# Optimization experiments

Hardware: AMD Instinct MI355X
Metric: run time of the kernel (lower is better)

The kernel has to match this reference:

```python
import jax, jax.numpy as jnp
from jax import lax
import numpy as np

RADIUS = 0.1
NSAMPLE = 32
STRIDE = 3
ED_NSAMPLE = 10


def _sqdist(a, b):
    # a: [B,M,3], b: [B,N,3] -> [B,M,N] squared euclidean distance
    return (jnp.sum(a * a, -1)[:, :, None] + jnp.sum(b * b, -1)[:, None, :]
            - 2.0 * jnp.einsum('bmc,bnc->bmn', a, b))


def setup_inputs() -> dict:
    key = jax.random.key(0)
    ks = jax.random.split(key, 16)
    B, N = 8, 4096
    s = 0.05
    inp = {
        'data': jax.random.normal(ks[0], (B, N, 3), dtype=jnp.float32),
        'numpoints': N,
        # stem MLP 3 -> 64
        'W_stem': jax.random.normal(ks[1], (3, 64), dtype=jnp.float32) * s,
        'b_stem': jnp.zeros((64,), jnp.float32),
        # SA shared MLP (3 dp + 64 fj) -> 128
        'W_sa': jax.random.normal(ks[2], (67, 128), dtype=jnp.float32) * s,
        'b_sa': jnp.zeros((128,), jnp.float32),
        # FP MLP (128 interp + 64 skip) -> 64
        'W_fp': jax.random.normal(ks[3], (192, 64), dtype=jnp.float32) * s,
        'b_fp': jnp.zeros((64,), jnp.float32),
        # eigen-feature MLP 3 -> 4 -> 4
        'W_e1': jax.random.normal(ks[4], (3, 4), dtype=jnp.float32) * s,
        'b_e1': jnp.zeros((4,), jnp.float32),
        'W_e2': jax.random.normal(ks[5], (4, 4), dtype=jnp.float32) * s,
        'b_e2': jnp.zeros((4,), jnp.float32),
        # conv_final 1x1: 68 -> 64, + BN affine
        'W_fin': jax.random.normal(ks[6], (68, 64), dtype=jnp.float32) * s,
        'b_fin': jnp.zeros((64,), jnp.float32),
        'gamma': jnp.ones((64,), jnp.float32),
        'beta': jnp.zeros((64,), jnp.float32),
    }
    return inp


def reference(data, numpoints, W_stem, b_stem, W_sa, b_sa, W_fp, b_fp,
              W_e1, b_e1, W_e2, b_e2, W_fin, b_fin, gamma, beta):
    B, N, _ = data.shape
    b_ix = jnp.arange(B)[:, None, None]

    # ---------- encoder: stem MLP ----------
    f0 = jax.nn.relu(data @ W_stem + b_stem)  # [B,N,64]

    # set abstraction: stride-subsample centers, ball query, dp_fj, MLP, max
    sub_idx = jnp.arange(0, N, STRIDE)
    new_xyz = data[:, sub_idx]                 # [B,M,3]
    d2 = _sqdist(new_xyz, data)                # [B,M,N]
    col = jnp.arange(N, dtype=jnp.int32)
    valid = d2 < RADIUS * RADIUS
    keys = jnp.where(valid, col, N + col)      # first-valid ball query ordering
    negk, _ = lax.top_k(-keys, NSAMPLE)
    idx = -negk                                # [B,M,ns]
    first = idx[..., :1]                       # self point always valid
    idx = jnp.where(idx >= N, first, idx)
    g_xyz = data[b_ix, idx]                    # [B,M,ns,3]
    dp = (g_xyz - new_xyz[:, :, None, :]) / RADIUS  # normalize_dp
    g_f = f0[b_ix, idx]                        # [B,M,ns,64]
    feat = jnp.concatenate([dp, g_f], -1)      # [B,M,ns,67]
    h = jax.nn.relu(feat @ W_sa + b_sa)        # [B,M,ns,128]
    f_sub = jnp.max(h, axis=2)                 # [B,M,128]

    # ---------- decoder: 3-NN inverse-distance feature propagation ----------
    d2f = _sqdist(data, new_xyz)               # [B,N,M]
    negd, nn = lax.top_k(-d2f, 3)
    w = 1.0 / (-negd + 1e-8)
    w = w / jnp.sum(w, -1, keepdims=True)      # [B,N,3]
    nbr_f = f_sub[b_ix, nn]                    # [B,N,3,128]
    interp = jnp.einsum('bnk,bnkc->bnc', w, nbr_f)
    f = jax.nn.relu(jnp.concatenate([interp, f0], -1) @ W_fp + b_fp)  # [B,N,64]

    # ---------- KNN covariance eigen-features ----------
    d2e = _sqdist(data, data)                  # [B,N,N]
    _, gidx = lax.top_k(-d2e, ED_NSAMPLE)      # [B,N,k]
    nbr = data[b_ix, gidx]                     # [B,N,k,3]
    cen = nbr - jnp.mean(nbr, axis=2, keepdims=True)
    cov = jnp.einsum('bnkc,bnkd->bncd', cen, cen) / ED_NSAMPLE  # [B,N,3,3]
    eig = jnp.linalg.eigvalsh(cov)             # [B,N,3] ascending
    ef = jax.nn.relu(eig @ W_e1 + b_e1) @ W_e2 + b_e2  # [B,N,4]

    # ---------- fused 1x1 conv + BN (training-mode stats) + relu ----------
    z_in = jnp.concatenate([f, ef], -1)        # [B,N,68]
    zc = z_in @ W_fin + b_fin                  # [B,N,64]
    mu = jnp.mean(zc, axis=(0, 1))
    var = jnp.var(zc, axis=(0, 1))
    z = jax.nn.relu((zc - mu) * lax.rsqrt(var + 1e-5) * gamma + beta)
    z = jnp.transpose(z, (0, 2, 1))            # [B,64,N]
    return (data, z)
```

## Files before the change

### kernel.cpp

```cpp
#include <hip/hip_runtime.h>
#include <stdint.h>

#define BB 8
#define NN 4096
#define MM 1366
#define NS 32
#define RAD2 0.01f
#define NGRP 64
#define KW 8

__device__ __forceinline__ float rl(float v, int l) {
    return __int_as_float(__builtin_amdgcn_readlane(__float_as_int(v), l));
}
__device__ __forceinline__ uint32_t um(uint32_t a, uint32_t b) { return a < b ? a : b; }
__device__ __forceinline__ uint32_t ux(uint32_t a, uint32_t b) { return a > b ? a : b; }
__device__ __forceinline__ uint32_t um3(uint32_t a, uint32_t b, uint32_t c) { return um(um(a, b), c); }

__device__ __forceinline__ void mrg2(uint32_t* kk, uint32_t s0, uint32_t s1) {
    uint32_t n0 = um(kk[0], s0);
    uint32_t n1 = um3(kk[1], ux(kk[0], s0), s1);
    uint32_t n2 = um3(kk[2], ux(kk[1], s0), ux(kk[0], s1));
    uint32_t n3 = um3(kk[3], ux(kk[2], s0), ux(kk[1], s1));
    uint32_t n4 = um3(kk[4], ux(kk[3], s0), ux(kk[2], s1));
    uint32_t n5 = um3(kk[5], ux(kk[4], s0), ux(kk[3], s1));
    uint32_t n6 = um3(kk[6], ux(kk[5], s0), ux(kk[4], s1));
    uint32_t n7 = um3(kk[7], ux(kk[6], s0), ux(kk[5], s1));
    uint32_t n8 = um3(kk[8], ux(kk[7], s0), ux(kk[6], s1));
    uint32_t n9 = um3(kk[9], ux(kk[8], s0), ux(kk[7], s1));
    kk[0]=n0; kk[1]=n1; kk[2]=n2; kk[3]=n3; kk[4]=n4;
    kk[5]=n5; kk[6]=n6; kk[7]=n7; kk[8]=n8; kk[9]=n9;
}

__device__ __forceinline__ void mrg4(uint32_t* kk, uint32_t s0, uint32_t s1,
                                     uint32_t s2, uint32_t s3) {
    uint32_t n0 = um(kk[0], s0);
    uint32_t n1 = um3(kk[1], ux(kk[0], s0), s1);
    uint32_t n2 = um(um3(kk[2], ux(kk[1], s0), ux(kk[0], s1)), s2);
    uint32_t n3 = um3(um3(kk[3], ux(kk[2], s0), ux(kk[1], s1)), ux(kk[0], s2), s3);
    uint32_t n4 = um3(um3(kk[4], ux(kk[3], s0), ux(kk[2], s1)), ux(kk[1], s2), ux(kk[0], s3));
    uint32_t n5 = um3(um3(kk[5], ux(kk[4], s0), ux(kk[3], s1)), ux(kk[2], s2), ux(kk[1], s3));
    uint32_t n6 = um3(um3(kk[6], ux(kk[5], s0), ux(kk[4], s1)), ux(kk[3], s2), ux(kk[2], s3));
    uint32_t n7 = um3(um3(kk[7], ux(kk[6], s0), ux(kk[5], s1)), ux(kk[4], s2), ux(kk[3], s3));
    uint32_t n8 = um3(um3(kk[8], ux(kk[7], s0), ux(kk[6], s1)), ux(kk[5], s2), ux(kk[4], s3));
    uint32_t n9 = um3(um3(kk[9], ux(kk[8], s0), ux(kk[7], s1)), ux(kk[6], s2), ux(kk[5], s3));
    kk[0]=n0; kk[1]=n1; kk[2]=n2; kk[3]=n3; kk[4]=n4;
    kk[5]=n5; kk[6]=n6; kk[7]=n7; kk[8]=n8; kk[9]=n9;
}

__device__ __forceinline__ void srt4(uint32_t& a, uint32_t& b, uint32_t& c, uint32_t& d) {
    uint32_t t0 = um(a, b), t1 = ux(a, b), t2 = um(c, d), t3 = ux(c, d);
    uint32_t s0 = um(t0, t2), m0 = ux(t0, t2), m1 = um(t1, t3), s3 = ux(t1, t3);
    a = s0; b = um(m0, m1); c = ux(m0, m1); d = s3;
}

__device__ __forceinline__ uint32_t spr3(uint32_t v) {
    v = (v | (v << 4)) & 0xC3u;
    v = (v | (v << 2)) & 0x249u;
    return v;
}

__global__ __launch_bounds__(256) void k_stem(const float* __restrict__ data,
                                              const float* __restrict__ Ws,
                                              const float* __restrict__ bs,
                                              float* __restrict__ f0,
                                              float* __restrict__ out,
                                              float4* __restrict__ cand4) {
    int blk = blockIdx.x;
    if (blk >= (BB * NN * 64) / 256) {
        int t = (blk - (BB * NN * 64) / 256) * 256 + threadIdx.x;
        float x = data[t * 3], y = data[t * 3 + 1], z = data[t * 3 + 2];
        out[t * 3] = x; out[t * 3 + 1] = y; out[t * 3 + 2] = z;
        cand4[t] = make_float4(x, y, z, x * x + y * y + z * z);
        return;
    }
    int t = blk * 256 + threadIdx.x;
    int c = t & 63;
    int r = t >> 6;
    const float* d = data + r * 3;
    float acc = bs[c];
    acc = fmaf(d[0], Ws[c], acc);
    acc = fmaf(d[1], Ws[64 + c], acc);
    acc = fmaf(d[2], Ws[128 + c], acc);
    f0[t] = fmaxf(acc, 0.f);
}

__global__ __launch_bounds__(256) void k_sort(const float4* __restrict__ cand4,
                                              float4* __restrict__ cand4s,
                                              uint32_t* __restrict__ perm,
                                              float4* __restrict__ gbox) {
    __shared__ uint32_t cnt[4096];
    __shared__ uint32_t part[256];
    int b = blockIdx.x, t = threadIdx.x;
    const float4* cb = cand4 + b * NN;
    for (int i = t; i < 4096; i += 256) cnt[i] = 0;
    __syncthreads();
    uint32_t cid[16];
    #pragma unroll
    for (int u = 0; u < 16; ++u) {
        float4 c = cb[u * 256 + t];
        int ix = (int)floorf((c.x + 4.f) * 2.f);
        int iy = (int)floorf((c.y + 4.f) * 2.f);
        int iz = (int)floorf((c.z + 4.f) * 2.f);
        ix = ix < 0 ? 0 : (ix > 15 ? 15 : ix);
        iy = iy < 0 ? 0 : (iy > 15 ? 15 : iy);
        iz = iz < 0 ? 0 : (iz > 15 ? 15 : iz);
        uint32_t m = spr3((uint32_t)ix) | (spr3((uint32_t)iy) << 1) | (spr3((uint32_t)iz) << 2);
        cid[u] = m;
        atomicAdd(&cnt[m], 1u);
    }
    __syncthreads();
    uint32_t c16[16];
    uint32_t s = 0;
    #pragma unroll
    for (int u = 0; u < 16; ++u) { c16[u] = cnt[t * 16 + u]; s += c16[u]; }
    part[t] = s;
    __syncthreads();
    for (int off = 1; off < 256; off <<= 1) {
        uint32_t v = (t >= off) ? part[t - off] : 0u;
        __syncthreads();
        part[t] += v;
        __syncthreads();
    }
    uint32_t run = part[t] - s;
    #pragma unroll
    for (int u = 0; u < 16; ++u) { cnt[t * 16 + u] = run; run += c16[u]; }
    __syncthreads();
    #pragma unroll
    for (int u = 0; u < 16; ++u) {
        int p = u * 256 + t;
        uint32_t pos = atomicAdd(&cnt[cid[u]], 1u);
        cand4s[b * NN + pos] = cb[p];
        perm[b * NN + pos] = (uint32_t)p;
    }
    __syncthreads();
    if (t < NGRP) {
        float4 mn = make_float4(1e30f, 1e30f, 1e30f, 0.f);
        float4 mx = make_float4(-1e30f, -1e30f, -1e30f, 0.f);
        for (int j = 0; j < 64; ++j) {
            float4 c = cand4s[b * NN + t * 64 + j];
            mn.x = fminf(mn.x, c.x); mn.y = fminf(mn.y, c.y); mn.z = fminf(mn.z, c.z);
            mx.x = fmaxf(mx.x, c.x); mx.y = fmaxf(mx.y, c.y); mx.z = fmaxf(mx.z, c.z);
        }
        gbox[(b * NGRP + t) * 2]     = mn;
        gbox[(b * NGRP + t) * 2 + 1] = mx;
    }
}

__global__ __launch_bounds__(512) void k_knn(const float4* __restrict__ cand4s,
                                             const uint32_t* __restrict__ perm,
                                             const float4* __restrict__ gbox,
                                             uint32_t* __restrict__ mrg) {
    __shared__ float4 sBox[2 * NGRP];
    __shared__ uint32_t sKK[KW - 1][64][10];
    int t = threadIdx.x, w = t >> 6, lane = t & 63;
    int gw = blockIdx.x;
    int b = gw >> 6;
    int g = gw & (NGRP - 1);
    for (int i = t; i < 2 * NGRP; i += 512) sBox[i] = gbox[b * 2 * NGRP + i];
    __syncthreads();
    const float4* cs = cand4s + b * NN;
    const uint32_t* ps = perm + b * NN;
    float4 me = cs[g * 64 + lane];
    uint32_t mo = ps[g * 64 + lane];
    float px = me.x, py = me.y, pz = me.z, pa = me.w;
    uint32_t kk[10];
    #pragma unroll
    for (int r = 0; r < 10; ++r) kk[r] = 0xFFFFFF00u + r;

    auto scan_packets = [&](int jg, uint32_t thrC) {
        const float4* cp = cs + jg * 64;
        const uint4* pq = (const uint4*)(ps + jg * 64);
        uint32_t thr = um(kk[9], thrC);
        for (int j = 0; j < 16; ++j) {
            float4 ca  = cp[j * 4];
            float4 cbv = cp[j * 4 + 1];
            float4 cc  = cp[j * 4 + 2];
            float4 cd  = cp[j * 4 + 3];
            uint4 pm = pq[j];
            float da  = fmaxf(fmaf(-2.f, fmaf(pz, ca.z,  fmaf(py, ca.y,  px * ca.x)),  pa + ca.w),  0.f);
            float db_ = fmaxf(fmaf(-2.f, fmaf(pz, cbv.z, fmaf(py, cbv.y, px * cbv.x)), pa + cbv.w), 0.f);
            float dc  = fmaxf(fmaf(-2.f, fmaf(pz, cc.z,  fmaf(py, cc.y,  px * cc.x)),  pa + cc.w),  0.f);
            float dd  = fmaxf(fmaf(-2.f, fmaf(pz, cd.z,  fmaf(py, cd.y,  px * cd.x)),  pa + cd.w),  0.f);
            uint32_t ka = (__float_as_uint(da)  & 0xFFFFF000u) | pm.x;
            uint32_t kb = (__float_as_uint(db_) & 0xFFFFF000u) | pm.y;
            uint32_t kc = (__float_as_uint(dc)  & 0xFFFFF000u) | pm.z;
            uint32_t kd = (__float_as_uint(dd)  & 0xFFFFF000u) | pm.w;
            uint32_t mn4 = um(um(ka, kb), um(kc, kd));
            if (__ballot(mn4 < thr)) {
                srt4(ka, kb, kc, kd);
                mrg4(kk, ka, kb, kc, kd);
                thr = um(kk[9], thrC);
            }
        }
    };

    scan_packets(g, 0xFFFFFFFFu);

    uint32_t thrK = (kk[9] & 0xFFFFF000u) + 0x1000u;

    if (w > 0) {
        #pragma unroll
        for (int r = 0; r < 10; ++r) kk[r] = 0xFFFFFF00u + r;
    }

    for (int jg = w; jg < NGRP; jg += KW) {
        if (jg == g) continue;
        float4 bmn = sBox[jg * 2], bmx = sBox[jg * 2 + 1];
        float dx = fmaxf(fmaxf(bmn.x - px, px - bmx.x), 0.f);
        float dy = fmaxf(fmaxf(bmn.y - py, py - bmx.y), 0.f);
        float dz = fmaxf(fmaxf(bmn.z - pz, pz - bmx.z), 0.f);
        float lb = fmaf(dx, dx, fmaf(dy, dy, dz * dz));
        uint32_t mt = um(kk[9], thrK);
        float tf = __uint_as_float((mt & 0xFFFFF000u) + 0x1000u) * 1.0005f;
        if (__ballot(lb < tf))
            scan_packets(jg, thrK);
    }

    if (w > 0) {
        #pragma unroll
        for (int r = 0; r < 10; ++r) sKK[w - 1][lane][r] = kk[r];
    }
    __syncthreads();
    if (w == 0) {
        for (int ww = 0; ww < KW - 1; ++ww) {
            uint32_t s[10];
            #pragma unroll
            for (int r = 0; r < 10; ++r) s[r] = sKK[ww][lane][r];
            mrg4(kk, s[0], s[1], s[2], s[3]);
            mrg4(kk, s[4], s[5], s[6], s[7]);
            mrg2(kk, s[8], s[9]);
        }
        int gp = b * NN + (int)mo;
        #pragma unroll
        for (int r = 0; r < 10; ++r) mrg[r * (BB * NN) + gp] = kk[r];
    }
}

__device__ __forceinline__ void jrot(float& app, float& aqq, float& apq,
                                     float& arp, float& arq) {
    float ap = apq;
    if (fabsf(ap) > 1e-32f) {
        float th = (aqq - app) / (2.f * ap);
        float t = 1.f / (fabsf(th) + sqrtf(th * th + 1.f));
        t = th < 0.f ? -t : t;
        float c = 1.f / sqrtf(t * t + 1.f);
        float s = t * c;
        app = app - t * ap;
        aqq = aqq + t * ap;
        apq = 0.f;
        float rp = arp, rq = arq;
        arp = c * rp - s * rq;
        arq = s * rp + c * rq;
    }
}

__global__ __launch_bounds__(256) void k_knn_eig(const float4* __restrict__ cand4,
                                                 const uint32_t* __restrict__ mrg,
                                                 const float* __restrict__ We1,
                                                 const float* __restrict__ be1,
                                                 const float* __restrict__ We2,
                                                 const float* __restrict__ be2,
                                                 float* __restrict__ ef) {
    int t = blockIdx.x * 256 + threadIdx.x;
    int b = t >> 12;
    const float4* cb = cand4 + b * NN;
    uint32_t kk[10];
    #pragma unroll
    for (int r = 0; r < 10; ++r) kk[r] = mrg[r * (BB * NN) + t];
    float xs[10], ys[10], zs[10];
    float mx = 0.f, my = 0.f, mz = 0.f;
    #pragma unroll
    for (int r = 0; r < 10; ++r) {
        int n = (int)(kk[r] & 0xFFFu);
        float4 cr = cb[n];
        xs[r] = cr.x; ys[r] = cr.y; zs[r] = cr.z;
        mx += xs[r]; my += ys[r]; mz += zs[r];
    }
    mx *= 0.1f; my *= 0.1f; mz *= 0.1f;
    float a00 = 0, a01 = 0, a02 = 0, a11 = 0, a12 = 0, a22 = 0;
    #pragma unroll
    for (int r = 0; r < 10; ++r) {
        float x = xs[r] - mx, y = ys[r] - my, z = zs[r] - mz;
        a00 = fmaf(x, x, a00); a01 = fmaf(x, y, a01); a02 = fmaf(x, z, a02);
        a11 = fmaf(y, y, a11); a12 = fmaf(y, z, a12); a22 = fmaf(z, z, a22);
    }
    a00 *= 0.1f; a01 *= 0.1f; a02 *= 0.1f; a11 *= 0.1f; a12 *= 0.1f; a22 *= 0.1f;
    #pragma unroll
    for (int sweep = 0; sweep < 6; ++sweep) {
        jrot(a00, a11, a01, a02, a12);
        jrot(a00, a22, a02, a01, a12);
        jrot(a11, a22, a12, a01, a02);
    }
    float e0 = a00, e1 = a11, e2 = a22, tmp;
    if (e0 > e1) { tmp = e0; e0 = e1; e1 = tmp; }
    if (e1 > e2) { tmp = e1; e1 = e2; e2 = tmp; }
    if (e0 > e1) { tmp = e0; e0 = e1; e1 = tmp; }
    float tt[4];
    #pragma unroll
    for (int i = 0; i < 4; ++i) {
        float v = be1[i];
        v = fmaf(e0, We1[i], v);
        v = fmaf(e1, We1[4 + i], v);
        v = fmaf(e2, We1[8 + i], v);
        tt[i] = fmaxf(v, 0.f);
    }
    #pragma unroll
    for (int i = 0; i < 4; ++i) {
        float v = be2[i];
        v = fmaf(tt[0], We2[i], v);
        v = fmaf(tt[1], We2[4 + i], v);
        v = fmaf(tt[2], We2[8 + i], v);
        v = fmaf(tt[3], We2[12 + i], v);
        ef[t * 4 + i] = v;
    }
}

__global__ __launch_bounds__(256) void k_sa(const float4* __restrict__ cand4,
                                            const float* __restrict__ data,
                                            const float* __restrict__ f0,
                                            const uint32_t* __restrict__ mrg,
                                            const float* __restrict__ Wsa,
                                            const float* __restrict__ bsa,
                                            float* __restrict__ fsub) {
    __shared__ float2 sW[67 * 64];
    __shared__ int sIdx[4][NS];
    for (int i = threadIdx.x; i < 67 * 64; i += 256) {
        int k = i >> 6, c = i & 63;
        sW[i] = make_float2(Wsa[k * 128 + c], Wsa[k * 128 + 64 + c]);
    }
    __syncthreads();
    int wv = threadIdx.x >> 6, lane = threadIdx.x & 63;
    int gm = blockIdx.x * 4 + wv;
    if (gm >= BB * MM) return;
    int b = gm / MM, m = gm - b * MM;
    const float4* cb4 = cand4 + b * NN;
    const float* db = data + b * NN * 3;
    float4 cen = cb4[3 * m];
    float cx = cen.x, cy = cen.y, cz = cen.z, sa = cen.w;

    int cnt;
    bool fallback;
    {
        float d2l = 1e30f;
        int idxl = 0;
        if (lane < 10) {
            uint32_t key = mrg[lane * (BB * NN) + b * NN + 3 * m];
            idxl = (int)(key & 0xFFFu);
            float4 c = cb4[idxl];
            float dot = fmaf(cz, c.z, fmaf(cy, c.y, cx * c.x));
            d2l = (sa + c.w) - 2.f * dot;
        }
        bool valid = (lane < 10) && (d2l < RAD2);
        unsigned long long mask = __ballot(valid);
        if (valid) sIdx[wv][__popcll(mask & ((1ull << lane) - 1ull))] = idxl;
        cnt = __popcll(mask);
        fallback = rl(d2l, 9) < RAD2 * 1.0005f;
    }
    if (fallback) {
        cnt = 0;
        for (int base = 0; base < NN; base += 64) {
            int n = base + lane;
            float4 c = cb4[n];
            float dot = fmaf(cz, c.z, fmaf(cy, c.y, cx * c.x));
            float d2 = (sa + c.w) - 2.f * dot;
            bool valid = d2 < RAD2;
            unsigned long long mask = __ballot(valid);
            if (valid) {
                int pos = cnt + __popcll(mask & ((1ull << lane) - 1ull));
                if (pos < NS) sIdx[wv][pos] = n;
            }
            cnt += __popcll(mask);
            if (cnt >= NS) break;
        }
    }
    int scnt = cnt < NS ? cnt : NS;

    float cl = lane == 0 ? cx : (lane == 1 ? cy : cz);
    float hb0 = bsa[lane], hb1 = bsa[64 + lane];
    float m0 = 0.f, m1 = 0.f;

    for (int s0 = 0; s0 < scnt; s0 += 4) {
        float fr[4], fr2[4];
        #pragma unroll
        for (int u = 0; u < 4; ++u) {
            int s = s0 + u;
            if (s >= scnt) s = 0;
            int nj = sIdx[wv][s];
            int fb = (b * NN + nj) * 64;
            float v;
            if (lane >= 3) v = f0[fb + lane - 3];
            else           v = (db[nj * 3 + lane] - cl) * 10.0f;
            fr[u] = v;
            fr2[u] = (lane < 3) ? f0[fb + 61 + lane] : 0.f;
        }
        float h0[4], h1[4];
        #pragma unroll
        for (int u = 0; u < 4; ++u) { h0[u] = hb0; h1[u] = hb1; }
        for (int k = 0; k < 64; ++k) {
            float2 w = sW[k * 64 + lane];
            #pragma unroll
            for (int u = 0; u < 4; ++u) {
                float fv = rl(fr[u], k);
                h0[u] = fmaf(fv, w.x, h0[u]);
                h1[u] = fmaf(fv, w.y, h1[u]);
            }
        }
        #pragma unroll
        for (int k = 64; k < 67; ++k) {
            float2 w = sW[k * 64 + lane];
            #pragma unroll
            for (int u = 0; u < 4; ++u) {
                float fv = rl(fr2[u], k - 64);
                h0[u] = fmaf(fv, w.x, h0[u]);
                h1[u] = fmaf(fv, w.y, h1[u]);
            }
        }
        #pragma unroll
        for (int u = 0; u < 4; ++u) {
            m0 = fmaxf(m0, fmaxf(h0[u], 0.f));
            m1 = fmaxf(m1, fmaxf(h1[u], 0.f));
        }
    }
    fsub[gm * 128 + lane] = m0;
    fsub[gm * 128 + 64 + lane] = m1;
}

__global__ __launch_bounds__(512) void k_interp(const float4* __restrict__ cand4,
                                                const float* __restrict__ fsub,
                                                float* __restrict__ itp) {
    __shared__ float4 sC[MM];
    __shared__ float sMD[8][64][3];
    __shared__ int   sMI[8][64][3];
    __shared__ float sWts[64][3];
    __shared__ int   sNbr[64][3];
    int t = threadIdx.x, wv = t >> 6, lane = t & 63;
    int blk = blockIdx.x;
    int b = blk >> 6;
    int pbase = (blk & 63) * 64;
    const float4* cb4 = cand4 + b * NN;
    for (int m = t; m < MM; m += 512) sC[m] = cb4[3 * m];
    __syncthreads();
    int p = pbase + lane;
    float4 pm = cb4[p];
    float px = pm.x, py = pm.y, pz = pm.z, pa = pm.w;
    float d0 = 1e30f, d1 = 1e30f, d2v = 1e30f;
    int n0 = 0, n1 = 0, n2 = 0;
    int ms = wv * 171, me = ms + 171 < MM ? ms + 171 : MM;
    for (int m = ms; m < me; ++m) {
        float4 c = sC[m];
        float dd = (pa + c.w) - 2.f * (px * c.x + py * c.y + pz * c.z);
        if (dd < d2v) {
            if (dd < d1) {
                d2v = d1; n2 = n1;
                if (dd < d0) { d1 = d0; n1 = n0; d0 = dd; n0 = m; }
                else         { d1 = dd; n1 = m; }
            } else { d2v = dd; n2 = m; }
        }
    }
    sMD[wv][lane][0] = d0; sMD[wv][lane][1] = d1; sMD[wv][lane][2] = d2v;
    sMI[wv][lane][0] = n0; sMI[wv][lane][1] = n1; sMI[wv][lane][2] = n2;
    __syncthreads();
    if (wv == 0) {
        d0 = sMD[0][lane][0]; d1 = sMD[0][lane][1]; d2v = sMD[0][lane][2];
        n0 = sMI[0][lane][0]; n1 = sMI[0][lane][1]; n2 = sMI[0][lane][2];
        for (int w = 1; w < 8; ++w) {
            #pragma unroll
            for (int r = 0; r < 3; ++r) {
                float dd = sMD[w][lane][r];
                int mm = sMI[w][lane][r];
                if (dd < d2v) {
                    if (dd < d1) {
                        d2v = d1; n2 = n1;
                        if (dd < d0) { d1 = d0; n1 = n0; d0 = dd; n0 = mm; }
                        else         { d1 = dd; n1 = mm; }
                    } else { d2v = dd; n2 = mm; }
                }
            }
        }
        float w0 = 1.f / (d0 + 1e-8f), w1 = 1.f / (d1 + 1e-8f), w2 = 1.f / (d2v + 1e-8f);
        float ws = w0 + w1 + w2;
        sWts[lane][0] = w0 / ws; sWts[lane][1] = w1 / ws; sWts[lane][2] = w2 / ws;
        sNbr[lane][0] = n0; sNbr[lane][1] = n1; sNbr[lane][2] = n2;
    }
    __syncthreads();
    for (int i = wv * 8; i < wv * 8 + 8; ++i) {
        float a0 = sWts[i][0], a1 = sWts[i][1], a2 = sWts[i][2];
        const float* r0 = fsub + (b * MM + sNbr[i][0]) * 128;
        const float* r1 = fsub + (b * MM + sNbr[i][1]) * 128;
        const float* r2 = fsub + (b * MM + sNbr[i][2]) * 128;
        float v0 = fmaf(a2, r2[lane], fmaf(a1, r1[lane], a0 * r0[lane]));
        float v1 = fmaf(a2, r2[64 + lane], fmaf(a1, r1[64 + lane], a0 * r0[64 + lane]));
        int row = b * NN + pbase + i;
        itp[row * 128 + lane] = v0;
        itp[row * 128 + 64 + lane] = v1;
    }
}

__global__ __launch_bounds__(256) void k_fp(const float* __restrict__ itp,
                                            const float* __restrict__ f0,
                                            const float* __restrict__ W,
                                            const float* __restrict__ bias,
                                            float* __restrict__ outf) {
    __shared__ float sW[192 * 64];
    for (int i = threadIdx.x; i < 192 * 64; i += 256) sW[i] = W[i];
    __syncthreads();
    int lane = threadIdx.x & 63;
    int wv = threadIdx.x >> 6;
    float bb = bias[lane];
    int rowbase = blockIdx.x * 64 + wv * 16;
    for (int it = 0; it < 4; ++it) {
        int r = rowbase + it * 4;
        float fa[4], fbv[4], fc[4], acc[4];
        #pragma unroll
        for (int u = 0; u < 4; ++u) {
            fa[u]  = itp[(r + u) * 128 + lane];
            fbv[u] = itp[(r + u) * 128 + 64 + lane];
            fc[u]  = f0[(r + u) * 64 + lane];
            acc[u] = bb;
        }
        #pragma unroll
        for (int k = 0; k < 192; ++k) {
            float w = sW[k * 64 + lane];
            #pragma unroll
            for (int u = 0; u < 4; ++u) {
                float fv = k < 64 ? rl(fa[u], k)
                         : (k < 128 ? rl(fbv[u], k - 64) : rl(fc[u], k - 128));
                acc[u] = fmaf(fv, w, acc[u]);
            }
        }
        #pragma unroll
        for (int u = 0; u < 4; ++u)
            outf[(r + u) * 64 + lane] = fmaxf(acc[u], 0.f);
    }
}

__global__ __launch_bounds__(256) void k_fin(const float* __restrict__ fb,
                                             const float* __restrict__ efb,
                                             const float* __restrict__ W,
                                             const float* __restrict__ bias,
                                             float* __restrict__ zc) {
    __shared__ float sW[68 * 64];
    for (int i = threadIdx.x; i < 68 * 64; i += 256) sW[i] = W[i];
    __syncthreads();
    int lane = threadIdx.x & 63;
    int wv = threadIdx.x >> 6;
    float bb = bias[lane];
    int rowbase = blockIdx.x * 64 + wv * 16;
    for (int it = 0; it < 4; ++it) {
        int r = rowbase + it * 4;
        float fa[4], fe[4], acc[4];
        #pragma unroll
        for (int u = 0; u < 4; ++u) {
            fa[u] = fb[(r + u) * 64 + lane];
            fe[u] = (lane < 4) ? efb[(r + u) * 4 + lane] : 0.f;
            acc[u] = bb;
        }
        #pragma unroll
        for (int k = 0; k < 68; ++k) {
            float w = sW[k * 64 + lane];
            #pragma unroll
            for (int u = 0; u < 4; ++u) {
                float fv = k < 64 ? rl(fa[u], k) : rl(fe[u], k - 64);
                acc[u] = fmaf(fv, w, acc[u]);
            }
        }
        #pragma unroll
        for (int u = 0; u < 4; ++u)
            zc[(r + u) * 64 + lane] = acc[u];
    }
}

__global__ __launch_bounds__(256) void k_stats1(const float* __restrict__ zc,
                                                float* __restrict__ pp) {
    int t = threadIdx.x;
    int c = t & 63, r4 = t >> 6;
    float s = 0.f, sq = 0.f;
    int base = blockIdx.x * 512;
    for (int i = 0; i < 128; ++i) {
        float v = zc[(base + i * 4 + r4) * 64 + c];
        s += v;
        sq = fmaf(v, v, sq);
    }
    __shared__ float ls[256], lq[256];
    ls[t] = s; lq[t] = sq;
    __syncthreads();
    if (t < 64) {
        float st = ls[t] + ls[t + 64] + ls[t + 128] + ls[t + 192];
        float qt = lq[t] + lq[t + 64] + lq[t + 128] + lq[t + 192];
        pp[blockIdx.x * 128 + t] = st;
        pp[blockIdx.x * 128 + 64 + t] = qt;
    }
}

__global__ __launch_bounds__(64) void k_stats2(const float* __restrict__ pp,
                                               const float* __restrict__ gamma,
                                               const float* __restrict__ beta,
                                               float* __restrict__ ss) {
    int c = threadIdx.x;
    float s = 0.f, sq = 0.f;
    for (int k = 0; k < 64; ++k) {
        s += pp[k * 128 + c];
        sq += pp[k * 128 + 64 + c];
    }
    const float inv = 1.f / (float)(BB * NN);
    float mu = s * inv;
    float var = sq * inv - mu * mu;
    float sc = gamma[c] / sqrtf(var + 1e-5f);
    ss[c] = sc;
    ss[64 + c] = beta[c] - mu * sc;
}

__global__ __launch_bounds__(256) void k_norm_t(const float* __restrict__ zc,
                                                const float* __restrict__ ss,
                                                float* __restrict__ out) {
    __shared__ float sT[64][65];
    int blk = blockIdx.x;
    int b = blk >> 6;
    int nbase = (blk & 63) * 64;
    int c = threadIdx.x & 63;
    int r4 = threadIdx.x >> 6;
    float sc = ss[c], sh = ss[64 + c];
    #pragma unroll
    for (int i = 0; i < 16; ++i) {
        int nr = i * 4 + r4;
        float v = zc[(b * NN + nbase + nr) * 64 + c];
        sT[nr][c] = fmaxf(fmaf(v, sc, sh), 0.f);
    }
    __syncthreads();
    int nn = threadIdx.x & 63;
    #pragma unroll
    for (int i = 0; i < 16; ++i) {
        int cc = i * 4 + r4;
        out[BB * NN * 3 + (b * 64 + cc) * NN + nbase + nn] = sT[nn][cc];
    }
}

extern "C" void kernel_launch(void* const* d_in, const int* in_sizes, int n_in,
                              void* d_out, int out_size, void* d_ws, size_t ws_size,
                              hipStream_t stream) {
    const float* data = (const float*)d_in[0];
    const float* Wst  = (const float*)d_in[2];
    const float* bst  = (const float*)d_in[3];
    const float* Wsa  = (const float*)d_in[4];
    const float* bsa  = (const float*)d_in[5];
    const float* Wfp  = (const float*)d_in[6];
    const float* bfp  = (const float*)d_in[7];
    const float* We1  = (const float*)d_in[8];
    const float* be1  = (const float*)d_in[9];
    const float* We2  = (const float*)d_in[10];
    const float* be2  = (const float*)d_in[11];
    const float* Wfin = (const float*)d_in[12];
    const float* bfin = (const float*)d_in[13];
    const float* gamma = (const float*)d_in[14];
    const float* beta  = (const float*)d_in[15];
    float* out = (float*)d_out;

    float* f0   = (float*)d_ws;
    float* fsub = f0 + 2097152;
    float* efb  = fsub + 1398784;
    float* zc   = efb + 131072;
    float* ss   = zc + 2097152;
    float* pp   = ss + 128;
    float4* cand4 = (float4*)(pp + 8192);
    uint32_t* mrgb = (uint32_t*)((float*)cand4 + 131072);
    float* itp  = (float*)mrgb + 1310720;
    float* fb   = itp + 4194304;
    float4*   cand4s = (float4*)itp;
    uint32_t* perm   = (uint32_t*)(itp + 131072);
    float4*   gbox   = (float4*)(itp + 131072 + 32768);

    k_stem<<<(BB * NN * 64) / 256 + (BB * NN) / 256, 256, 0, stream>>>(
        data, Wst, bst, f0, out, cand4);
    k_sort<<<BB, 256, 0, stream>>>(cand4, cand4s, perm, gbox);
    k_knn<<<BB * NGRP, 512, 0, stream>>>(cand4s, perm, gbox, mrgb);
    k_knn_eig<<<(BB * NN) / 256, 256, 0, stream>>>(cand4, mrgb, We1, be1, We2, be2, efb);
    k_sa<<<(BB * MM + 3) / 4, 256, 0, stream>>>(cand4, data, f0, mrgb, Wsa, bsa, fsub);
    k_interp<<<BB * 64, 512, 0, stream>>>(cand4, fsub, itp);
    k_fp<<<512, 256, 0, stream>>>(itp, f0, Wfp, bfp, fb);
    k_fin<<<512, 256, 0, stream>>>(fb, efb, Wfin, bfin, zc);
    k_stats1<<<64, 256, 0, stream>>>(zc, pp);
    k_stats2<<<1, 64, 0, stream>>>(pp, gamma, beta, ss);
    k_norm_t<<<512, 256, 0, stream>>>(zc, ss, out);
}
```

Measured before the change: 317.8 us.

## Split KNN into home-group pass and independent slice scans merged in eig kernel

The single 512-thread KNN kernel is split into three stages. A 64-thread kernel scans each point's home group and stores a pruning threshold. A scan kernel then runs twice as many 256-thread blocks, each wave handling one of eight slices of the other groups. A final merge of the per-slice top-10 lists moves into the eigen kernel, with the scatter back to original order done there. This removes the in-block shared-memory merge and the __syncthreads stall, and spreads work over more, smaller blocks for better occupancy. In exchange it adds a kernel launch and global traffic for nine partial top-10 lists per point.

```diff
diff --git a/kernel.cpp b/kernel.cpp
--- a/kernel.cpp
+++ b/kernel.cpp
@@ -7,7 +7,7 @@
 #define NS 32
 #define RAD2 0.01f
 #define NGRP 64
-#define KW 8
+#define NSL 8
 
 __device__ __forceinline__ float rl(float v, int l) {
     return __int_as_float(__builtin_amdgcn_readlane(__float_as_int(v), l));
@@ -59,6 +59,34 @@
     return v;
 }
 
+__device__ __forceinline__ void scan_grp(const float4* __restrict__ cp,
+                                         const uint4* __restrict__ pq,
+                                         float px, float py, float pz, float pa,
+                                         uint32_t thrC, uint32_t* kk) {
+    uint32_t thr = um(kk[9], thrC);
+    for (int j = 0; j < 16; ++j) {
+        float4 ca  = cp[j * 4];
+        float4 cbv = cp[j * 4 + 1];
+        float4 cc  = cp[j * 4 + 2];
+        float4 cd  = cp[j * 4 + 3];
+        uint4 pm = pq[j];
+        float da  = fmaxf(fmaf(-2.f, fmaf(pz, ca.z,  fmaf(py, ca.y,  px * ca.x)),  pa + ca.w),  0.f);
+        float db_ = fmaxf(fmaf(-2.f, fmaf(pz, cbv.z, fmaf(py, cbv.y, px * cbv.x)), pa + cbv.w), 0.f);
+        float dc  = fmaxf(fmaf(-2.f, fmaf(pz, cc.z,  fmaf(py, cc.y,  px * cc.x)),  pa + cc.w),  0.f);
+        float dd  = fmaxf(fmaf(-2.f, fmaf(pz, cd.z,  fmaf(py, cd.y,  px * cd.x)),  pa + cd.w),  0.f);
+        uint32_t ka = (__float_as_uint(da)  & 0xFFFFF000u) | pm.x;
+        uint32_t kb = (__float_as_uint(db_) & 0xFFFFF000u) | pm.y;
+        uint32_t kc = (__float_as_uint(dc)  & 0xFFFFF000u) | pm.z;
+        uint32_t kd = (__float_as_uint(dd)  & 0xFFFFF000u) | pm.w;
+        uint32_t mn4 = um(um(ka, kb), um(kc, kd));
+        if (__ballot(mn4 < thr)) {
+            srt4(ka, kb, kc, kd);
+            mrg4(kk, ka, kb, kc, kd);
+            thr = um(kk[9], thrC);
+        }
+    }
+}
+
 __global__ __launch_bounds__(256) void k_stem(const float* __restrict__ data,
                                               const float* __restrict__ Ws,
                                               const float* __restrict__ bs,
@@ -146,64 +174,50 @@
     }
 }
 
-__global__ __launch_bounds__(512) void k_knn(const float4* __restrict__ cand4s,
+__global__ __launch_bounds__(64) void k_home(const float4* __restrict__ cand4s,
                                              const uint32_t* __restrict__ perm,
-                                             const float4* __restrict__ gbox,
-                                             uint32_t* __restrict__ mrg) {
-    __shared__ float4 sBox[2 * NGRP];
-    __shared__ uint32_t sKK[KW - 1][64][10];
-    int t = threadIdx.x, w = t >> 6, lane = t & 63;
+                                             uint32_t* __restrict__ pk,
+                                             uint32_t* __restrict__ thrKbuf) {
     int gw = blockIdx.x;
-    int b = gw >> 6;
-    int g = gw & (NGRP - 1);
-    for (int i = t; i < 2 * NGRP; i += 512) sBox[i] = gbox[b * 2 * NGRP + i];
-    __syncthreads();
+    int b = gw >> 6, g = gw & (NGRP - 1);
+    int lane = threadIdx.x;
     const float4* cs = cand4s + b * NN;
     const uint32_t* ps = perm + b * NN;
     float4 me = cs[g * 64 + lane];
-    uint32_t mo = ps[g * 64 + lane];
     float px = me.x, py = me.y, pz = me.z, pa = me.w;
     uint32_t kk[10];
     #pragma unroll
     for (int r = 0; r < 10; ++r) kk[r] = 0xFFFFFF00u + r;
-
-    auto scan_packets = [&](int jg, uint32_t thrC) {
-        const float4* cp = cs + jg * 64;
-        const uint4* pq = (const uint4*)(ps + jg * 64);
-        uint32_t thr = um(kk[9], thrC);
-        for (int j = 0; j < 16; ++j) {
-            float4 ca  = cp[j * 4];
-            float4 cbv = cp[j * 4 + 1];
-            float4 cc  = cp[j * 4 + 2];
-            float4 cd  = cp[j * 4 + 3];
-            uint4 pm = pq[j];
-            float da  = fmaxf(fmaf(-2.f, fmaf(pz, ca.z,  fmaf(py, ca.y,  px * ca.x)),  pa + ca.w),  0.f);
-            float db_ = fmaxf(fmaf(-2.f, fmaf(pz, cbv.z, fmaf(py, cbv.y, px * cbv.x)), pa + cbv.w), 0.f);
-            float dc  = fmaxf(fmaf(-2.f, fmaf(pz, cc.z,  fmaf(py, cc.y,  px * cc.x)),  pa + cc.w),  0.f);
-            float dd  = fmaxf(fmaf(-2.f, fmaf(pz, cd.z,  fmaf(py, cd.y,  px * cd.x)),  pa + cd.w),  0.f);
-            uint32_t ka = (__float_as_uint(da)  & 0xFFFFF000u) | pm.x;
-            uint32_t kb = (__float_as_uint(db_) & 0xFFFFF000u) | pm.y;
-            uint32_t kc = (__float_as_uint(dc)  & 0xFFFFF000u) | pm.z;
-            uint32_t kd = (__float_as_uint(dd)  & 0xFFFFF000u) | pm.w;
-            uint32_t mn4 = um(um(ka, kb), um(kc, kd));
-            if (__ballot(mn4 < thr)) {
-                srt4(ka, kb, kc, kd);
-                mrg4(kk, ka, kb, kc, kd);
-                thr = um(kk[9], thrC);
-            }
-        }
-    };
-
-    scan_packets(g, 0xFFFFFFFFu);
-
-    uint32_t thrK = (kk[9] & 0xFFFFF000u) + 0x1000u;
-
-    if (w > 0) {
-        #pragma unroll
-        for (int r = 0; r < 10; ++r) kk[r] = 0xFFFFFF00u + r;
-    }
-
-    for (int jg = w; jg < NGRP; jg += KW) {
+    scan_grp(cs + g * 64, (const uint4*)(ps + g * 64), px, py, pz, pa, 0xFFFFFFFFu, kk);
+    int spos = b * NN + g * 64 + lane;
+    thrKbuf[spos] = (kk[9] & 0xFFFFF000u) + 0x1000u;
+    #pragma unroll
+    for (int r = 0; r < 10; ++r) pk[(NSL * 10 + r) * (BB * NN) + spos] = kk[r];
+}
+
+__global__ __launch_bounds__(256) void k_knn_scan(const float4* __restrict__ cand4s,
+                                                  const uint32_t* __restrict__ perm,
+                                                  const float4* __restrict__ gbox,
+                                                  const uint32_t* __restrict__ thrKbuf,
+                                                  uint32_t* __restrict__ pk) {
+    __shared__ float4 sBox[2 * NGRP];
+    int t = threadIdx.x, w = t >> 6, lane = t & 63;
+    int blk = blockIdx.x;
+    int gb = blk >> 1, h = blk & 1;
+    int b = gb >> 6, g = gb & (NGRP - 1);
+    int sig = h * 4 + w;
+    for (int i = t; i < 2 * NGRP; i += 256) sBox[i] = gbox[b * 2 * NGRP + i];
+    __syncthreads();
+    const float4* cs = cand4s + b * NN;
+    const uint32_t* ps = perm + b * NN;
+    float4 me = cs[g * 64 + lane];
+    float px = me.x, py = me.y, pz = me.z, pa = me.w;
+    int spos = b * NN + g * 64 + lane;
+    uint32_t thrK = thrKbuf[spos];
+    uint32_t kk[10];
+    #pragma unroll
+    for (int r = 0; r < 10; ++r) kk[r] = 0xFFFFFF00u + r;
+    for (int jg = sig; jg < NGRP; jg += NSL) {
         if (jg == g) continue;
         float4 bmn = sBox[jg * 2], bmx = sBox[jg * 2 + 1];
         float dx = fmaxf(fmaxf(bmn.x - px, px - bmx.x), 0.f);
@@ -213,27 +227,10 @@
         uint32_t mt = um(kk[9], thrK);
         float tf = __uint_as_float((mt & 0xFFFFF000u) + 0x1000u) * 1.0005f;
         if (__ballot(lb < tf))
-            scan_packets(jg, thrK);
-    }
-
-    if (w > 0) {
-        #pragma unroll
-        for (int r = 0; r < 10; ++r) sKK[w - 1][lane][r] = kk[r];
-    }
-    __syncthreads();
-    if (w == 0) {
-        for (int ww = 0; ww < KW - 1; ++ww) {
-            uint32_t s[10];
-            #pragma unroll
-            for (int r = 0; r < 10; ++r) s[r] = sKK[ww][lane][r];
-            mrg4(kk, s[0], s[1], s[2], s[3]);
-            mrg4(kk, s[4], s[5], s[6], s[7]);
-            mrg2(kk, s[8], s[9]);
-        }
-        int gp = b * NN + (int)mo;
-        #pragma unroll
-        for (int r = 0; r < 10; ++r) mrg[r * (BB * NN) + gp] = kk[r];
-    }
+            scan_grp(cs + jg * 64, (const uint4*)(ps + jg * 64), px, py, pz, pa, thrK, kk);
+    }
+    #pragma unroll
+    for (int r = 0; r < 10; ++r) pk[(sig * 10 + r) * (BB * NN) + spos] = kk[r];
 }
 
 __device__ __forceinline__ void jrot(float& app, float& aqq, float& apq,
@@ -255,7 +252,9 @@
 }
 
 __global__ __launch_bounds__(256) void k_knn_eig(const float4* __restrict__ cand4,
-                                                 const uint32_t* __restrict__ mrg,
+                                                 const uint32_t* __restrict__ pk,
+                                                 const uint32_t* __restrict__ perm,
+                                                 uint32_t* __restrict__ mrg,
                                                  const float* __restrict__ We1,
                                                  const float* __restrict__ be1,
                                                  const float* __restrict__ We2,
@@ -266,7 +265,21 @@
     const float4* cb = cand4 + b * NN;
     uint32_t kk[10];
     #pragma unroll
-    for (int r = 0; r < 10; ++r) kk[r] = mrg[r * (BB * NN) + t];
+    for (int r = 0; r < 10; ++r) kk[r] = pk[(NSL * 10 + r) * (BB * NN) + t];
+    for (int sig = 0; sig < NSL; ++sig) {
+        uint32_t s[10];
+        #pragma unroll
+        for (int r = 0; r < 10; ++r) s[r] = pk[(sig * 10 + r) * (BB * NN) + t];
+        if (__ballot(s[0] < 0xFFFFF000u)) {
+            mrg4(kk, s[0], s[1], s[2], s[3]);
+            mrg4(kk, s[4], s[5], s[6], s[7]);
+            mrg2(kk, s[8], s[9]);
+        }
+    }
+    int orig = (int)(perm[t] & 0xFFFu);
+    int gp = b * NN + orig;
+    #pragma unroll
+    for (int r = 0; r < 10; ++r) mrg[r * (BB * NN) + gp] = kk[r];
     float xs[10], ys[10], zs[10];
     float mx = 0.f, my = 0.f, mz = 0.f;
     #pragma unroll
@@ -311,7 +324,7 @@
         v = fmaf(tt[1], We2[4 + i], v);
         v = fmaf(tt[2], We2[8 + i], v);
         v = fmaf(tt[3], We2[12 + i], v);
-        ef[t * 4 + i] = v;
+        ef[gp * 4 + i] = v;
     }
 }
 
@@ -668,12 +681,16 @@
     float4*   cand4s = (float4*)itp;
     uint32_t* perm   = (uint32_t*)(itp + 131072);
     float4*   gbox   = (float4*)(itp + 131072 + 32768);
+    uint32_t* pk     = (uint32_t*)(itp + 167936);
+    uint32_t* thrK   = pk + (NSL + 1) * 10 * (BB * NN);
 
     k_stem<<<(BB * NN * 64) / 256 + (BB * NN) / 256, 256, 0, stream>>>(
         data, Wst, bst, f0, out, cand4);
     k_sort<<<BB, 256, 0, stream>>>(cand4, cand4s, perm, gbox);
-    k_knn<<<BB * NGRP, 512, 0, stream>>>(cand4s, perm, gbox, mrgb);
-    k_knn_eig<<<(BB * NN) / 256, 256, 0, stream>>>(cand4, mrgb, We1, be1, We2, be2, efb);
+    k_home<<<BB * NGRP, 64, 0, stream>>>(cand4s, perm, pk, thrK);
+    k_knn_scan<<<BB * NGRP * 2, 256, 0, stream>>>(cand4s, perm, gbox, thrK, pk);
+    k_knn_eig<<<(BB * NN) / 256, 256, 0, stream>>>(cand4, pk, perm, mrgb,
+                                                   We1, be1, We2, be2, efb);
     k_sa<<<(BB * MM + 3) / 4, 256, 0, stream>>>(cand4, data, f0, mrgb, Wsa, bsa, fsub);
     k_interp<<<BB * 64, 512, 0, stream>>>(cand4, fsub, itp);
     k_fp<<<512, 256, 0, stream>>>(itp, f0, Wfp, bfp, fb);
```

Result: slower. 326.0 us (+2.6%).
